# Optimization experiments

Hardware: AMD Instinct MI355X
Metric: run time of the kernel (lower is better)

Reference implementation:

```python
import jax, jax.numpy as jnp
import numpy as np

N_NODES = 12288
N_FEATURES = 256
KEY_DIM = 128
N_GRAPHS = 192


def setup_inputs() -> dict:
    key = jax.random.key(0)
    k1, k2, k3, k4, k5 = jax.random.split(key, 5)
    node_out = jax.random.normal(k1, (N_NODES, N_FEATURES), dtype=jnp.float32)
    batch = jnp.sort(jax.random.randint(k2, (N_NODES,), 0, N_GRAPHS, dtype=jnp.int64))
    # xavier_uniform: limit = sqrt(6 / (fan_in + fan_out))
    lim_qk = float(np.sqrt(6.0 / (N_FEATURES + KEY_DIM)))
    lim_v = float(np.sqrt(6.0 / (N_FEATURES + N_FEATURES)))
    query_weight = jax.random.uniform(k3, (N_FEATURES, KEY_DIM), jnp.float32, -lim_qk, lim_qk)
    key_weight = jax.random.uniform(k4, (N_FEATURES, KEY_DIM), jnp.float32, -lim_qk, lim_qk)
    value_weight = jax.random.uniform(k5, (N_FEATURES, N_FEATURES), jnp.float32, -lim_v, lim_v)
    return {
        "node_out": node_out,
        "batch": batch,
        "query_weight": query_weight,
        "key_weight": key_weight,
        "value_weight": value_weight,
    }


def reference(node_out, batch, query_weight, key_weight, value_weight):
    n_features = node_out.shape[1]
    Q = node_out @ query_weight            # [N, K]
    K = node_out @ key_weight              # [N, K]
    V = node_out @ value_weight            # [N, F]
    # NOTE: original scales by sqrt(n_features), not sqrt(key_dim)
    scores = (Q @ K.T) / jnp.sqrt(jnp.asarray(n_features, dtype=Q.dtype))  # [N, N]
    mask = batch[:, None] == batch[None, :]  # block-diagonal per-graph mask
    scores = jnp.where(mask, scores, -jnp.inf)
    attn = jax.nn.softmax(scores, axis=-1)   # every row has >=1 valid entry
    context = attn @ V                        # [N, F]
    return jax.ops.segment_sum(context, batch, num_segments=N_GRAPHS)  # [G, F]
```

## Files before the change

kernel.cpp:

```cpp
#include <hip/hip_runtime.h>
#include <hip/hip_bf16.h>

#define N_NODES  12288
#define N_FEAT   256
#define KDIM     128
#define N_GRAPHS 192
#define NMAX     112
#define KSTRIDE_U 68
#define XS_STRIDE_U 132

#define WS_STARTS 0
#define WS_WBUF   1024
#define WS_QB     (WS_WBUF + N_NODES * 4)
#define WS_KB     (WS_QB + N_NODES * 64 * 4)
#define WS_WT     (WS_KB + N_NODES * 64 * 4)

typedef __bf16 bf16x8 __attribute__((ext_vector_type(8)));
typedef float  f32x4  __attribute__((ext_vector_type(4)));

__device__ __forceinline__ unsigned bf16_rne(float f) {
  unsigned u = __float_as_uint(f);
  return (u + 0x7FFFu + ((u >> 16) & 1u)) >> 16;
}
__device__ __forceinline__ unsigned pack_bf16(float lo, float hi) {
  return bf16_rne(lo) | (bf16_rne(hi) << 16);
}
__device__ __forceinline__ float bf_lo(unsigned u) { return __uint_as_float(u << 16); }
__device__ __forceinline__ float bf_hi(unsigned u) { return __uint_as_float(u & 0xFFFF0000u); }

__global__ __launch_bounds__(64) void wt_prep_k(const float* __restrict__ Wq,
                                                const float* __restrict__ Wk,
                                                const int* __restrict__ batch,
                                                unsigned* __restrict__ Wt,
                                                int* __restrict__ starts) {
  const int n = blockIdx.x;
  const int t = threadIdx.x;
  const float* src = (n < KDIM) ? (Wq + n) : (Wk + (n - KDIM));
  float f0 = src[(4 * t + 0) * KDIM];
  float f1 = src[(4 * t + 1) * KDIM];
  float f2 = src[(4 * t + 2) * KDIM];
  float f3 = src[(4 * t + 3) * KDIM];
  Wt[n * 128 + 2 * t]     = pack_bf16(f0, f1);
  Wt[n * 128 + 2 * t + 1] = pack_bf16(f2, f3);

  if (t == 0 && n <= N_GRAPHS) {
    int lo = 0, hi = N_NODES;
    while (lo < hi) {
      int mid = (lo + hi) >> 1;
      if (batch[mid] < n) lo = mid + 1; else hi = mid;
    }
    starts[n] = lo;
  }
}

__global__ __launch_bounds__(512) void attn_fused_k(const float* __restrict__ X,
                                                    const int* __restrict__ starts,
                                                    const unsigned* __restrict__ Wt,
                                                    const float* __restrict__ Wv,
                                                    float* __restrict__ out,
                                                    unsigned* __restrict__ Qb,
                                                    unsigned* __restrict__ Kb,
                                                    float* __restrict__ wbuf) {
  __shared__ unsigned Xs_u[NMAX * XS_STRIDE_U];
  __shared__ unsigned Qs_u[NMAX * KSTRIDE_U];
  __shared__ unsigned Ks_u[NMAX * KSTRIDE_U];
  __shared__ float    w_lds[8][NMAX];
  __shared__ float    red[2][256];
  __shared__ float    Us[256];

  const int tid  = threadIdx.x;
  const int lane = tid & 63;
  const int wv   = tid >> 6;
  const int l15  = lane & 15;
  const int quad = lane >> 4;
  const int g    = blockIdx.x;

  const int i0 = starts[g];
  const int n  = starts[g + 1] - i0;
  const float BIG = 1e30f;
  const bool fast = (n <= NMAX);

  bf16x8 bq0[8], bq1[8];
  {
    const unsigned* w0 = &Wt[(size_t)((2 * wv + 0) * 16 + l15) * 128 + quad * 4];
    const unsigned* w1 = &Wt[(size_t)((2 * wv + 1) * 16 + l15) * 128 + quad * 4];
#pragma unroll
    for (int ks = 0; ks < 8; ks++) {
      bq0[ks] = *(const bf16x8*)&w0[ks * 16];
      bq1[ks] = *(const bf16x8*)&w1[ks * 16];
    }
  }
  unsigned* dst_lds   = (wv < 4) ? Qs_u : Ks_u;
  const float scale   = (wv < 4) ? 0.0625f : 1.0f;
  const int cb0 = ((2 * wv + 0) & 7) * 16;
  const int cb1 = ((2 * wv + 1) & 7) * 16;

  if (fast) {
    const int ns   = (n + 15) >> 4;
    const int npad = ns * 16;

    for (int idx = tid; idx < npad * 16; idx += 512) {
      int row = idx >> 4, seg = idx & 15;
      unsigned* dst = &Xs_u[row * XS_STRIDE_U + seg * 8];
      if (row < n) {
        const float* xp = &X[(size_t)(i0 + row) * N_FEAT + seg * 16];
        float4 a = *(const float4*)xp;
        float4 b = *(const float4*)(xp + 4);
        float4 c = *(const float4*)(xp + 8);
        float4 d = *(const float4*)(xp + 12);
        *(uint4*)dst       = make_uint4(pack_bf16(a.x, a.y), pack_bf16(a.z, a.w),
                                        pack_bf16(b.x, b.y), pack_bf16(b.z, b.w));
        *(uint4*)(dst + 4) = make_uint4(pack_bf16(c.x, c.y), pack_bf16(c.z, c.w),
                                        pack_bf16(d.x, d.y), pack_bf16(d.z, d.w));
      } else {
        *(uint4*)dst       = make_uint4(0u, 0u, 0u, 0u);
        *(uint4*)(dst + 4) = make_uint4(0u, 0u, 0u, 0u);
      }
    }
    __syncthreads();

    for (int s = 0; s < ns; s++) {
      f32x4 acc0 = (f32x4){0.f, 0.f, 0.f, 0.f};
      f32x4 acc1 = (f32x4){0.f, 0.f, 0.f, 0.f};
#pragma unroll
      for (int ks = 0; ks < 8; ks++) {
        bf16x8 a = *(const bf16x8*)&Xs_u[(s * 16 + l15) * XS_STRIDE_U + ks * 16 + quad * 4];
        acc0 = __builtin_amdgcn_mfma_f32_16x16x32_bf16(a, bq0[ks], acc0, 0, 0, 0);
        acc1 = __builtin_amdgcn_mfma_f32_16x16x32_bf16(a, bq1[ks], acc1, 0, 0, 0);
      }
#pragma unroll
      for (int e = 0; e < 4; e++) {
        const int row = s * 16 + quad * 4 + e;
        unsigned b0 = bf16_rne(acc0[e] * scale);
        unsigned p0 = __shfl_xor((int)b0, 1);
        unsigned b1 = bf16_rne(acc1[e] * scale);
        unsigned p1 = __shfl_xor((int)b1, 1);
        if ((lane & 1) == 0) {
          dst_lds[row * KSTRIDE_U + ((cb0 + l15) >> 1)] = b0 | (p0 << 16);
          dst_lds[row * KSTRIDE_U + ((cb1 + l15) >> 1)] = b1 | (p1 << 16);
        }
      }
    }
    __syncthreads();

    float wl[7];
#pragma unroll
    for (int f = 0; f < 7; f++) wl[f] = 0.f;

    if (wv < ns) {
      const int s = wv;
      const int arow = min(s * 16 + l15, n - 1);
      bf16x8 au[4];
#pragma unroll
      for (int ks = 0; ks < 4; ks++)
        au[ks] = *(const bf16x8*)&Qs_u[arow * KSTRIDE_U + ks * 16 + quad * 4];

      f32x4 acc[7];
#pragma unroll
      for (int f = 0; f < 7; f++) acc[f] = (f32x4){0.f, 0.f, 0.f, 0.f};
#pragma unroll
      for (int f = 0; f < 7; f++) {
#pragma unroll
        for (int ks = 0; ks < 4; ks++) {
          bf16x8 bu = *(const bf16x8*)&Ks_u[(f * 16 + l15) * KSTRIDE_U + ks * 16 + quad * 4];
          acc[f] = __builtin_amdgcn_mfma_f32_16x16x32_bf16(au[ks], bu, acc[f], 0, 0, 0);
        }
      }
#pragma unroll
      for (int f = 0; f < 7; f++)
        if (f * 16 + l15 >= n) {
          acc[f][0] = -BIG; acc[f][1] = -BIG; acc[f][2] = -BIG; acc[f][3] = -BIG;
        }

#pragma unroll
      for (int e = 0; e < 4; e++) {
        float m = -BIG;
#pragma unroll
        for (int f = 0; f < 7; f++) m = fmaxf(m, acc[f][e]);
        m = fmaxf(m, __shfl_xor(m, 1));
        m = fmaxf(m, __shfl_xor(m, 2));
        m = fmaxf(m, __shfl_xor(m, 4));
        m = fmaxf(m, __shfl_xor(m, 8));
        float p[7], l = 0.f;
#pragma unroll
        for (int f = 0; f < 7; f++) { p[f] = __expf(acc[f][e] - m); l += p[f]; }
        l += __shfl_xor(l, 1);
        l += __shfl_xor(l, 2);
        l += __shfl_xor(l, 4);
        l += __shfl_xor(l, 8);
        const int row = s * 16 + quad * 4 + e;
        float inv = (row < n) ? (1.f / l) : 0.f;
#pragma unroll
        for (int f = 0; f < 7; f++) wl[f] = fmaf(p[f], inv, wl[f]);
      }
    }

#pragma unroll
    for (int f = 0; f < 7; f++) {
      wl[f] += __shfl_xor(wl[f], 16);
      wl[f] += __shfl_xor(wl[f], 32);
    }
    if (lane < 16) {
#pragma unroll
      for (int f = 0; f < 7; f++) w_lds[wv][f * 16 + lane] = wl[f];
    }
    __syncthreads();

    if (tid < NMAX) {
      float t = 0.f;
#pragma unroll
      for (int k = 0; k < 8; k++) t += w_lds[k][tid];
      w_lds[0][tid] = t;
    }
    __syncthreads();
  } else {
    for (int idx = tid; idx < n; idx += 512) wbuf[i0 + idx] = 0.f;

    for (int c0 = 0; c0 < n; c0 += NMAX) {
      const int cn  = min(NMAX, n - c0);
      const int cns = (cn + 15) >> 4;
      __syncthreads();
      for (int idx = tid; idx < cns * 16 * 16; idx += 512) {
        int row = idx >> 4, seg = idx & 15;
        unsigned* dst = &Xs_u[row * XS_STRIDE_U + seg * 8];
        if (row < cn) {
          const float* xp = &X[(size_t)(i0 + c0 + row) * N_FEAT + seg * 16];
          float4 a = *(const float4*)xp;
          float4 b = *(const float4*)(xp + 4);
          float4 c = *(const float4*)(xp + 8);
          float4 d = *(const float4*)(xp + 12);
          *(uint4*)dst       = make_uint4(pack_bf16(a.x, a.y), pack_bf16(a.z, a.w),
                                          pack_bf16(b.x, b.y), pack_bf16(b.z, b.w));
          *(uint4*)(dst + 4) = make_uint4(pack_bf16(c.x, c.y), pack_bf16(c.z, c.w),
                                          pack_bf16(d.x, d.y), pack_bf16(d.z, d.w));
        } else {
          *(uint4*)dst       = make_uint4(0u, 0u, 0u, 0u);
          *(uint4*)(dst + 4) = make_uint4(0u, 0u, 0u, 0u);
        }
      }
      __syncthreads();
      unsigned* dstg = (wv < 4) ? Qb : Kb;
      for (int s = 0; s < cns; s++) {
        f32x4 acc0 = (f32x4){0.f, 0.f, 0.f, 0.f};
        f32x4 acc1 = (f32x4){0.f, 0.f, 0.f, 0.f};
#pragma unroll
        for (int ks = 0; ks < 8; ks++) {
          bf16x8 a = *(const bf16x8*)&Xs_u[(s * 16 + l15) * XS_STRIDE_U + ks * 16 + quad * 4];
          acc0 = __builtin_amdgcn_mfma_f32_16x16x32_bf16(a, bq0[ks], acc0, 0, 0, 0);
          acc1 = __builtin_amdgcn_mfma_f32_16x16x32_bf16(a, bq1[ks], acc1, 0, 0, 0);
        }
#pragma unroll
        for (int e = 0; e < 4; e++) {
          const int row = s * 16 + quad * 4 + e;
          unsigned b0 = bf16_rne(acc0[e] * scale);
          unsigned p0 = __shfl_xor((int)b0, 1);
          unsigned b1 = bf16_rne(acc1[e] * scale);
          unsigned p1 = __shfl_xor((int)b1, 1);
          if ((lane & 1) == 0 && row < cn) {
            dstg[(size_t)(i0 + c0 + row) * 64 + ((cb0 + l15) >> 1)] = b0 | (p0 << 16);
            dstg[(size_t)(i0 + c0 + row) * 64 + ((cb1 + l15) >> 1)] = b1 | (p1 << 16);
          }
        }
      }
    }
    __threadfence();
    __syncthreads();

    for (int lr = wv; lr < n; lr += 8) {
      const uint4* qp4 = (const uint4*)&Qb[(size_t)(i0 + lr) * 64];
      float m_run = -BIG, l_run = 0.f;
      for (int jb = 0; jb < n; jb += 64) {
        int j = jb + lane;
        int jc = min(j, n - 1);
        const uint4* kp4 = (const uint4*)&Kb[(size_t)(i0 + jc) * 64];
        float s = 0.f;
        for (int c = 0; c < 16; c++) {
          uint4 Q1 = qp4[c];
          uint4 K1 = kp4[c];
          s = fmaf(bf_lo(Q1.x), bf_lo(K1.x), s); s = fmaf(bf_hi(Q1.x), bf_hi(K1.x), s);
          s = fmaf(bf_lo(Q1.y), bf_lo(K1.y), s); s = fmaf(bf_hi(Q1.y), bf_hi(K1.y), s);
          s = fmaf(bf_lo(Q1.z), bf_lo(K1.z), s); s = fmaf(bf_hi(Q1.z), bf_hi(K1.z), s);
          s = fmaf(bf_lo(Q1.w), bf_lo(K1.w), s); s = fmaf(bf_hi(Q1.w), bf_hi(K1.w), s);
        }
        if (j >= n) s = -BIG;
        float mc = s;
        for (int off = 32; off; off >>= 1) mc = fmaxf(mc, __shfl_xor(mc, off));
        float m_new = fmaxf(m_run, mc);
        float lc = __expf(s - m_new);
        for (int off = 32; off; off >>= 1) lc += __shfl_xor(lc, off);
        l_run = l_run * __expf(m_run - m_new) + lc;
        m_run = m_new;
      }
      float inv = 1.f / l_run;
      for (int jb = 0; jb < n; jb += 64) {
        int j = jb + lane;
        int jc = min(j, n - 1);
        const uint4* kp4 = (const uint4*)&Kb[(size_t)(i0 + jc) * 64];
        float s = 0.f;
        for (int c = 0; c < 16; c++) {
          uint4 Q1 = qp4[c];
          uint4 K1 = kp4[c];
          s = fmaf(bf_lo(Q1.x), bf_lo(K1.x), s); s = fmaf(bf_hi(Q1.x), bf_hi(K1.x), s);
          s = fmaf(bf_lo(Q1.y), bf_lo(K1.y), s); s = fmaf(bf_hi(Q1.y), bf_hi(K1.y), s);
          s = fmaf(bf_lo(Q1.z), bf_lo(K1.z), s); s = fmaf(bf_hi(Q1.z), bf_hi(K1.z), s);
          s = fmaf(bf_lo(Q1.w), bf_lo(K1.w), s); s = fmaf(bf_hi(Q1.w), bf_hi(K1.w), s);
        }
        if (j < n) atomicAdd(&wbuf[i0 + j], __expf(s - m_run) * inv);
      }
    }
    __threadfence();
    __syncthreads();
  }

  const int f  = tid & 255;
  const int jp = tid >> 8;
  float u0 = 0.f, u1 = 0.f, u2 = 0.f, u3 = 0.f;
  if (fast) {
    int j = jp;
    for (; j + 6 < n; j += 8) {
      u0 = fmaf(w_lds[0][j],     X[(size_t)(i0 + j) * N_FEAT + f], u0);
      u1 = fmaf(w_lds[0][j + 2], X[(size_t)(i0 + j + 2) * N_FEAT + f], u1);
      u2 = fmaf(w_lds[0][j + 4], X[(size_t)(i0 + j + 4) * N_FEAT + f], u2);
      u3 = fmaf(w_lds[0][j + 6], X[(size_t)(i0 + j + 6) * N_FEAT + f], u3);
    }
    for (; j < n; j += 2)
      u0 = fmaf(w_lds[0][j], X[(size_t)(i0 + j) * N_FEAT + f], u0);
  } else {
    for (int j = jp; j < n; j += 2) {
      float wj = atomicAdd(&wbuf[i0 + j], 0.f);
      u0 = fmaf(wj, X[(size_t)(i0 + j) * N_FEAT + f], u0);
    }
  }
  red[jp][f] = (u0 + u1) + (u2 + u3);
  __syncthreads();
  if (jp == 0) Us[f] = red[0][f] + red[1][f];
  __syncthreads();

  const int k0 = jp * 128;
  const float* wp = Wv + (size_t)k0 * N_FEAT + f;
  const float* us = &Us[k0];
  float a0 = 0.f, a1 = 0.f, a2 = 0.f, a3 = 0.f;
#pragma unroll 8
  for (int k = 0; k < 128; k += 4) {
    a0 = fmaf(us[k],     wp[(size_t)k * N_FEAT], a0);
    a1 = fmaf(us[k + 1], wp[(size_t)(k + 1) * N_FEAT], a1);
    a2 = fmaf(us[k + 2], wp[(size_t)(k + 2) * N_FEAT], a2);
    a3 = fmaf(us[k + 3], wp[(size_t)(k + 3) * N_FEAT], a3);
  }
  __syncthreads();
  red[jp][f] = (a0 + a1) + (a2 + a3);
  __syncthreads();
  if (jp == 0) out[g * N_FEAT + f] = red[0][f] + red[1][f];
}

extern "C" void kernel_launch(void* const* d_in, const int* in_sizes, int n_in,
                              void* d_out, int out_size, void* d_ws, size_t ws_size,
                              hipStream_t stream) {
  const float* X     = (const float*)d_in[0];
  const int*   batch = (const int*)d_in[1];
  const float* Wq    = (const float*)d_in[2];
  const float* Wk    = (const float*)d_in[3];
  const float* Wv    = (const float*)d_in[4];
  float* out = (float*)d_out;

  char* ws = (char*)d_ws;
  int*      starts = (int*)(ws + WS_STARTS);
  float*    wbuf   = (float*)(ws + WS_WBUF);
  unsigned* Qb     = (unsigned*)(ws + WS_QB);
  unsigned* Kb     = (unsigned*)(ws + WS_KB);
  unsigned* Wt     = (unsigned*)(ws + WS_WT);

  wt_prep_k<<<256, 64, 0, stream>>>(Wq, Wk, batch, Wt, starts);
  attn_fused_k<<<N_GRAPHS, 512, 0, stream>>>(X, starts, Wt, Wv, out, Qb, Kb, wbuf);
}
```

Baseline: 86.67 us.

## Fold weight prep and segment search into main attention kernel

Removes the separate prep kernel that transposed and bf16-packed Wq/Wk and computed graph start offsets. Each block now loads and packs its weight fragments straight from the fp32 weights, and finds its segment bounds with a wave-parallel 64-way ballot search over the sorted batch array. This saves one kernel launch and the dependency between the two kernels. In exchange every block does redundant strided global reads of Wq/Wk and the search work itself.

```diff
diff --git a/kernel.cpp b/kernel.cpp
--- a/kernel.cpp
+++ b/kernel.cpp
@@ -9,11 +9,9 @@
 #define KSTRIDE_U 68
 #define XS_STRIDE_U 132
 
-#define WS_STARTS 0
 #define WS_WBUF   1024
 #define WS_QB     (WS_WBUF + N_NODES * 4)
 #define WS_KB     (WS_QB + N_NODES * 64 * 4)
-#define WS_WT     (WS_KB + N_NODES * 64 * 4)
 
 typedef __bf16 bf16x8 __attribute__((ext_vector_type(8)));
 typedef float  f32x4  __attribute__((ext_vector_type(4)));
@@ -28,34 +26,30 @@
 __device__ __forceinline__ float bf_lo(unsigned u) { return __uint_as_float(u << 16); }
 __device__ __forceinline__ float bf_hi(unsigned u) { return __uint_as_float(u & 0xFFFF0000u); }
 
-__global__ __launch_bounds__(64) void wt_prep_k(const float* __restrict__ Wq,
-                                                const float* __restrict__ Wk,
-                                                const int* __restrict__ batch,
-                                                unsigned* __restrict__ Wt,
-                                                int* __restrict__ starts) {
-  const int n = blockIdx.x;
-  const int t = threadIdx.x;
-  const float* src = (n < KDIM) ? (Wq + n) : (Wk + (n - KDIM));
-  float f0 = src[(4 * t + 0) * KDIM];
-  float f1 = src[(4 * t + 1) * KDIM];
-  float f2 = src[(4 * t + 2) * KDIM];
-  float f3 = src[(4 * t + 3) * KDIM];
-  Wt[n * 128 + 2 * t]     = pack_bf16(f0, f1);
-  Wt[n * 128 + 2 * t + 1] = pack_bf16(f2, f3);
-
-  if (t == 0 && n <= N_GRAPHS) {
-    int lo = 0, hi = N_NODES;
-    while (lo < hi) {
-      int mid = (lo + hi) >> 1;
-      if (batch[mid] < n) lo = mid + 1; else hi = mid;
-    }
-    starts[n] = lo;
-  }
+__device__ __forceinline__ int lb64(const int* __restrict__ batch, int target, int lane) {
+  int lo = 0, hi = N_NODES;
+  while (hi > lo) {
+    int w = hi - lo;
+    int step = (w + 63) >> 6;
+    int idx = lo + lane * step;
+    bool lt = (idx < hi) && (batch[idx] < target);
+    unsigned long long b = __ballot(lt);
+    int c = __popcll(b);
+    if (c == 0) {
+      hi = lo;
+    } else {
+      int nhi = lo + c * step;
+      lo = lo + (c - 1) * step + 1;
+      hi = (nhi < hi) ? nhi : hi;
+    }
+  }
+  return lo;
 }
 
 __global__ __launch_bounds__(512) void attn_fused_k(const float* __restrict__ X,
-                                                    const int* __restrict__ starts,
-                                                    const unsigned* __restrict__ Wt,
+                                                    const int* __restrict__ batch,
+                                                    const float* __restrict__ Wq,
+                                                    const float* __restrict__ Wk,
                                                     const float* __restrict__ Wv,
                                                     float* __restrict__ out,
                                                     unsigned* __restrict__ Qb,
@@ -74,24 +68,35 @@
   const int l15  = lane & 15;
   const int quad = lane >> 4;
   const int g    = blockIdx.x;
-
-  const int i0 = starts[g];
-  const int n  = starts[g + 1] - i0;
   const float BIG = 1e30f;
-  const bool fast = (n <= NMAX);
-
+
+  union U8 { unsigned u[4]; bf16x8 v; };
   bf16x8 bq0[8], bq1[8];
   {
-    const unsigned* w0 = &Wt[(size_t)((2 * wv + 0) * 16 + l15) * 128 + quad * 4];
-    const unsigned* w1 = &Wt[(size_t)((2 * wv + 1) * 16 + l15) * 128 + quad * 4];
+    const float* wsrc = (wv < 4) ? Wq : Wk;
+    const int c0 = (wv & 3) * 32 + l15;
 #pragma unroll
     for (int ks = 0; ks < 8; ks++) {
-      bq0[ks] = *(const bf16x8*)&w0[ks * 16];
-      bq1[ks] = *(const bf16x8*)&w1[ks * 16];
-    }
-  }
-  unsigned* dst_lds   = (wv < 4) ? Qs_u : Ks_u;
-  const float scale   = (wv < 4) ? 0.0625f : 1.0f;
+      U8 t0, t1;
+#pragma unroll
+      for (int p = 0; p < 4; p++) {
+        const int k = ks * 32 + quad * 8 + 2 * p;
+        const float* r0p = wsrc + (size_t)k * KDIM;
+        const float* r1p = wsrc + (size_t)(k + 1) * KDIM;
+        t0.u[p] = pack_bf16(r0p[c0], r1p[c0]);
+        t1.u[p] = pack_bf16(r0p[c0 + 16], r1p[c0 + 16]);
+      }
+      bq0[ks] = t0.v;
+      bq1[ks] = t1.v;
+    }
+  }
+
+  const int i0 = lb64(batch, g, lane);
+  const int n  = lb64(batch, g + 1, lane) - i0;
+  const bool fast = (n <= NMAX);
+
+  unsigned* dst_lds = (wv < 4) ? Qs_u : Ks_u;
+  const float scale = (wv < 4) ? 0.0625f : 1.0f;
   const int cb0 = ((2 * wv + 0) & 7) * 16;
   const int cb1 = ((2 * wv + 1) & 7) * 16;
 
@@ -364,12 +369,9 @@
   float* out = (float*)d_out;
 
   char* ws = (char*)d_ws;
-  int*      starts = (int*)(ws + WS_STARTS);
-  float*    wbuf   = (float*)(ws + WS_WBUF);
-  unsigned* Qb     = (unsigned*)(ws + WS_QB);
-  unsigned* Kb     = (unsigned*)(ws + WS_KB);
-  unsigned* Wt     = (unsigned*)(ws + WS_WT);
-
-  wt_prep_k<<<256, 64, 0, stream>>>(Wq, Wk, batch, Wt, starts);
-  attn_fused_k<<<N_GRAPHS, 512, 0, stream>>>(X, starts, Wt, Wv, out, Qb, Kb, wbuf);
-}
+  float*    wbuf = (float*)(ws + WS_WBUF);
+  unsigned* Qb   = (unsigned*)(ws + WS_QB);
+  unsigned* Kb   = (unsigned*)(ws + WS_KB);
+
+  attn_fused_k<<<N_GRAPHS, 512, 0, stream>>>(X, batch, Wq, Wk, Wv, out, Qb, Kb, wbuf);
+}
```

New measurement: 82.19 us. 1.05x faster.
